# Kernel optimization log

Measured on AMD Instinct MI355X. Metric: run time of the kernel, lower is better.

Reference implementation:

```python
import jax, jax.numpy as jnp
import numpy as np

EPS = 1e-05


def project_to_poincare_ball(v, eps=EPS):
    # clip norm to < 1 - eps
    norm = jnp.linalg.norm(v, axis=-1, keepdims=True)
    scale = jnp.minimum((1.0 - eps) / (norm + 1e-10), 1.0)
    return v * scale


def setup_inputs() -> dict:
    key = jax.random.key(0)
    k1, k2 = jax.random.split(key)
    B, S, D, V = 2, 2048, 512, 32000
    # scale by 0.02 so typical norms (~0.45) lie inside the unit ball
    hidden_states = jax.random.normal(k1, (B, S, D), dtype=jnp.float32) * 0.02
    weight = jax.random.normal(k2, (V, D), dtype=jnp.float32) * 0.02
    return {"hidden_states": hidden_states, "weight": weight}


def reference(hidden_states, weight):
    eps = EPS
    B, S, D = hidden_states.shape
    x = hidden_states.reshape(-1, D)                 # (N, D)
    x = project_to_poincare_ball(x, eps)
    y = project_to_poincare_ball(weight, eps)        # (V, D)

    x_norm_sq = jnp.sum(x * x, axis=-1, keepdims=True)   # (N, 1)
    y_norm_sq = jnp.sum(y * y, axis=-1)                  # (V,)

    # torch.cdist(p=2, use_mm_for_euclid_dist): ||x-y|| via mm expansion,
    # clamped at 0 before sqrt. NOTE: original code names this diff_norm_sq
    # but it is the (unsquared) distance -- reproduced faithfully.
    sq = x_norm_sq + y_norm_sq[None, :] - 2.0 * (x @ y.T)   # (N, V)
    dist = jnp.sqrt(jnp.maximum(sq, 0.0))

    denom = (1.0 - x_norm_sq) * (1.0 - y_norm_sq)[None, :]  # (N, V)
    argument = 1.0 + 2.0 * dist / (denom + eps)
    argument = jnp.maximum(argument, 1.0 + eps)
    distances = jnp.arccosh(argument)                       # (N, V)

    logits = -distances
    return logits.reshape(B, S, -1)
```

## Files before the change

### kernel.cpp

```cpp
#include <hip/hip_runtime.h>
#include <hip/hip_bf16.h>

#define D_DIM 512
#define EPS 1e-5f
#define BM 256
#define BN 256
#define BK 32
#define KT 16

typedef __attribute__((ext_vector_type(8))) short bf16x8;
typedef __attribute__((ext_vector_type(4))) float f32x4;

__device__ __forceinline__ unsigned short f2bf(float f) {
  unsigned int u = __float_as_uint(f);
  u += 0x7FFFu + ((u >> 16) & 1u);
  return (unsigned short)(u >> 16);
}

__global__ __launch_bounds__(256) void prep_rows2(
    const float* __restrict__ x, const float* __restrict__ w,
    unsigned short* __restrict__ Xbf, unsigned short* __restrict__ Ybf,
    float* __restrict__ xnsq, float* __restrict__ ynsq, int N, int total)
{
  int row  = blockIdx.x * 4 + (threadIdx.x >> 6);
  int lane = threadIdx.x & 63;
  if (row >= total) return;

  const float* src; unsigned short* dst; float* nsq; int r;
  if (row < N) { src = x; dst = Xbf; nsq = xnsq; r = row; }
  else         { src = w; dst = Ybf; nsq = ynsq; r = row - N; }

  const float4* s = (const float4*)(src + (size_t)r * D_DIM);
  float4 v0 = s[lane];
  float4 v1 = s[lane + 64];
  float ss = v0.x*v0.x + v0.y*v0.y + v0.z*v0.z + v0.w*v0.w
           + v1.x*v1.x + v1.y*v1.y + v1.z*v1.z + v1.w*v1.w;
  #pragma unroll
  for (int off = 32; off; off >>= 1) ss += __shfl_xor(ss, off);

  float norm  = sqrtf(ss);
  float scale = fminf((1.0f - EPS) / (norm + 1e-10f), 1.0f);
  if (lane == 0) nsq[r] = ss * scale * scale;

  ushort4 o0, o1;
  o0.x = f2bf(v0.x * scale); o0.y = f2bf(v0.y * scale);
  o0.z = f2bf(v0.z * scale); o0.w = f2bf(v0.w * scale);
  o1.x = f2bf(v1.x * scale); o1.y = f2bf(v1.y * scale);
  o1.z = f2bf(v1.z * scale); o1.w = f2bf(v1.w * scale);

  ushort4* dp = (ushort4*)(dst + (size_t)r * D_DIM);
  dp[lane]      = o0;
  dp[lane + 64] = o1;
}

__global__ __launch_bounds__(512, 2) void hyp_gemm(
    const unsigned short* __restrict__ Xbf, const unsigned short* __restrict__ Ybf,
    const float* __restrict__ xnsq, const float* __restrict__ ynsq,
    float* __restrict__ out, int N, int V)
{
  __shared__ __attribute__((aligned(16))) unsigned short regions[2][2 * BM * BK];

  int bid = blockIdx.x;
  int local = bid >> 3;
  int bn = local >> 1;
  int bm = (bid & 7) * 2 + (local & 1);

  int tid  = threadIdx.x;
  int wid  = tid >> 6;
  int lane = tid & 63;
  int wm = wid >> 2, wn = wid & 3;

  size_t a_row0 = (size_t)bm * BM;
  size_t b_row0 = (size_t)bn * BN;

  int rA = tid >> 2;
  int sw = (tid & 3) ^ ((tid >> 2) & 3);
  auto STAGE = [&](int reg, int kt) {
    int k0 = kt * BK;
    char* base = (char*)&regions[reg][0];
    #pragma unroll
    for (int j = 0; j < 2; ++j) {
      const unsigned short* g = Xbf + (a_row0 + j * 128 + rA) * D_DIM + k0 + sw * 8;
      char* l = base + j * 8192 + wid * 1024;
      __builtin_amdgcn_global_load_lds(
          (const __attribute__((address_space(1))) void*)g,
          (__attribute__((address_space(3))) void*)l, 16, 0, 0);
    }
    #pragma unroll
    for (int j = 0; j < 2; ++j) {
      const unsigned short* g = Ybf + (b_row0 + j * 128 + rA) * D_DIM + k0 + sw * 8;
      char* l = base + 16384 + j * 8192 + wid * 1024;
      __builtin_amdgcn_global_load_lds(
          (const __attribute__((address_space(1))) void*)g,
          (__attribute__((address_space(3))) void*)l, 16, 0, 0);
    }
  };

  f32x4 acc[8][4] = {};
  int r = lane & 15;
  int h = lane >> 4;
  int slotoff = ((h ^ (r & 3)) * 8);

  STAGE(0, 0);

  #pragma unroll
  for (int t = 0; t < KT; ++t) {
    const unsigned short* sA = &regions[t & 1][0];
    const unsigned short* sB = sA + BM * BK;

    asm volatile("s_waitcnt vmcnt(0)" ::: "memory");
    __builtin_amdgcn_sched_barrier(0);
    __builtin_amdgcn_s_barrier();
    __builtin_amdgcn_sched_barrier(0);

    bf16x8 a[8], b0, b1;
    #pragma unroll
    for (int m = 0; m < 8; ++m)
      a[m] = *(const bf16x8*)&sA[(wm * 128 + m * 16 + r) * BK + slotoff];
    b0 = *(const bf16x8*)&sB[(wn * 64 + 0 * 16 + r) * BK + slotoff];
    b1 = *(const bf16x8*)&sB[(wn * 64 + 1 * 16 + r) * BK + slotoff];

    if (t + 1 < KT) STAGE((t + 1) & 1, t + 1);

    __builtin_amdgcn_sched_barrier(0);
    __builtin_amdgcn_s_barrier();
    __builtin_amdgcn_sched_barrier(0);
    __builtin_amdgcn_s_setprio(1);
    #pragma unroll
    for (int m = 0; m < 8; ++m) {
      acc[m][0] = __builtin_amdgcn_mfma_f32_16x16x32_bf16(b0, a[m], acc[m][0], 0, 0, 0);
      acc[m][1] = __builtin_amdgcn_mfma_f32_16x16x32_bf16(b1, a[m], acc[m][1], 0, 0, 0);
    }
    __builtin_amdgcn_s_setprio(0);

    __builtin_amdgcn_sched_barrier(0);
    __builtin_amdgcn_s_barrier();
    __builtin_amdgcn_sched_barrier(0);
    bf16x8 b2 = *(const bf16x8*)&sB[(wn * 64 + 2 * 16 + r) * BK + slotoff];
    bf16x8 b3 = *(const bf16x8*)&sB[(wn * 64 + 3 * 16 + r) * BK + slotoff];

    __builtin_amdgcn_sched_barrier(0);
    __builtin_amdgcn_s_barrier();
    __builtin_amdgcn_sched_barrier(0);
    __builtin_amdgcn_s_setprio(1);
    #pragma unroll
    for (int m = 0; m < 8; ++m) {
      acc[m][2] = __builtin_amdgcn_mfma_f32_16x16x32_bf16(b2, a[m], acc[m][2], 0, 0, 0);
      acc[m][3] = __builtin_amdgcn_mfma_f32_16x16x32_bf16(b3, a[m], acc[m][3], 0, 0, 0);
    }
    __builtin_amdgcn_s_setprio(0);
  }

  __syncthreads();
  float* epi = (float*)&regions[0][0] + wid * (16 * 68);

  int jr = r;
  float xnv[8], cmv[8];
  #pragma unroll
  for (int m = 0; m < 8; ++m) {
    float xn = xnsq[bm * BM + wm * 128 + m * 16 + jr];
    xnv[m] = xn;
    cmv[m] = 2.0f * __builtin_amdgcn_rcpf(1.0f - xn);
  }
  f32x4 ynv[4], rdy[4];
  #pragma unroll
  for (int n = 0; n < 4; ++n) {
    f32x4 y4 = *(const f32x4*)&ynsq[bn * BN + wn * 64 + n * 16 + h * 4];
    ynv[n] = y4;
    #pragma unroll
    for (int q = 0; q < 4; ++q) rdy[n][q] = __builtin_amdgcn_rcpf(1.0f - y4[q]);
  }

  size_t out_row0 = (size_t)bm * BM + wm * 128;
  int    out_col0 = bn * BN + wn * 64;

  #pragma unroll
  for (int m = 0; m < 8; ++m) {
    float xn = xnv[m], cm = cmv[m];
    #pragma unroll
    for (int n = 0; n < 4; ++n) {
      f32x4 f;
      #pragma unroll
      for (int q = 0; q < 4; ++q) {
        float dot  = acc[m][n][q];
        float sq   = fmaxf(xn + ynv[n][q] - 2.0f * dot, 0.0f);
        float dist = __builtin_amdgcn_sqrtf(sq);
        float arg  = fmaf(dist * cm, rdy[n][q], 1.0f);
        arg = fmaxf(arg, 1.0f + EPS);
        float t2 = __builtin_amdgcn_sqrtf(fmaf(arg, arg, -1.0f));
        f[q] = -__logf(arg + t2);
      }
      *(f32x4*)&epi[jr * 68 + n * 16 + h * 4] = f;
    }
    #pragma unroll
    for (int k = 0; k < 4; ++k) {
      int xl = k * 4 + h;
      f32x4 f = *(const f32x4*)&epi[xl * 68 + jr * 4];
      size_t rg = out_row0 + m * 16 + xl;
      int    cg = out_col0 + jr * 4;
      __builtin_nontemporal_store(f, (f32x4*)(out + rg * (size_t)V + cg));
    }
  }
}

extern "C" void kernel_launch(void* const* d_in, const int* in_sizes, int n_in,
                              void* d_out, int out_size, void* d_ws, size_t ws_size,
                              hipStream_t stream) {
  const float* x = (const float*)d_in[0];
  const float* w = (const float*)d_in[1];
  float* out = (float*)d_out;

  int N = in_sizes[0] / D_DIM;
  int V = in_sizes[1] / D_DIM;

  char* ws = (char*)d_ws;
  unsigned short* Xbf = (unsigned short*)ws;
  size_t xbf_bytes = (size_t)N * D_DIM * 2;
  unsigned short* Ybf = (unsigned short*)(ws + xbf_bytes);
  size_t ybf_bytes = (size_t)V * D_DIM * 2;
  float* xnsq = (float*)(ws + xbf_bytes + ybf_bytes);
  float* ynsq = xnsq + N;

  int total = N + V;
  prep_rows2<<<dim3((total + 3) / 4), dim3(256), 0, stream>>>(
      x, w, Xbf, Ybf, xnsq, ynsq, N, total);

  int nwg = (N / BM) * (V / BN);
  hyp_gemm<<<dim3(nwg), dim3(512), 0, stream>>>(Xbf, Ybf, xnsq, ynsq, out, N, V);
}
```

Measured before the change: 241.6 us.

## Triple-buffer LDS tiles with two-stage prefetch and split A/B staging

Moves the GEMM main loop from double to triple LDS buffering, prefetching the tile two steps ahead. Waits use a partial vmcnt so the tile in flight is not drained each iteration. The A and B staging loads are now issued at two separate points in the loop to spread memory traffic across the MFMA phases. Per-block LDS grows from 64 KB to 96 KB, so two 512-thread blocks may no longer fit on one CU, which can halve occupancy.

```diff
diff --git a/kernel.cpp b/kernel.cpp
--- a/kernel.cpp
+++ b/kernel.cpp
@@ -58,7 +58,7 @@
     const float* __restrict__ xnsq, const float* __restrict__ ynsq,
     float* __restrict__ out, int N, int V)
 {
-  __shared__ __attribute__((aligned(16))) unsigned short regions[2][2 * BM * BK];
+  __shared__ __attribute__((aligned(16))) unsigned short regions[3][2 * BM * BK];
 
   int bid = blockIdx.x;
   int local = bid >> 3;
@@ -73,23 +73,31 @@
   size_t a_row0 = (size_t)bm * BM;
   size_t b_row0 = (size_t)bn * BN;
 
-  int rA = tid >> 2;
-  int sw = (tid & 3) ^ ((tid >> 2) & 3);
-  auto STAGE = [&](int reg, int kt) {
+  auto STAGE_A = [&](int reg, int kt) {
     int k0 = kt * BK;
     char* base = (char*)&regions[reg][0];
     #pragma unroll
-    for (int j = 0; j < 2; ++j) {
-      const unsigned short* g = Xbf + (a_row0 + j * 128 + rA) * D_DIM + k0 + sw * 8;
-      char* l = base + j * 8192 + wid * 1024;
+    for (int i = 0; i < 2; ++i) {
+      int c = i * 512 + tid;
+      int row = c >> 2;
+      int sw = (c & 3) ^ (row & 3);
+      const unsigned short* g = Xbf + (a_row0 + row) * D_DIM + k0 + sw * 8;
+      char* l = base + (size_t)(i * 512 + wid * 64) * 16;
       __builtin_amdgcn_global_load_lds(
           (const __attribute__((address_space(1))) void*)g,
           (__attribute__((address_space(3))) void*)l, 16, 0, 0);
     }
-    #pragma unroll
-    for (int j = 0; j < 2; ++j) {
-      const unsigned short* g = Ybf + (b_row0 + j * 128 + rA) * D_DIM + k0 + sw * 8;
-      char* l = base + 16384 + j * 8192 + wid * 1024;
+  };
+  auto STAGE_B = [&](int reg, int kt) {
+    int k0 = kt * BK;
+    char* base = (char*)&regions[reg][0] + 2 * BM * BK;
+    #pragma unroll
+    for (int i = 0; i < 2; ++i) {
+      int c = i * 512 + tid;
+      int row = c >> 2;
+      int sw = (c & 3) ^ (row & 3);
+      const unsigned short* g = Ybf + (b_row0 + row) * D_DIM + k0 + sw * 8;
+      char* l = base + (size_t)(i * 512 + wid * 64) * 16;
       __builtin_amdgcn_global_load_lds(
           (const __attribute__((address_space(1))) void*)g,
           (__attribute__((address_space(3))) void*)l, 16, 0, 0);
@@ -99,16 +107,21 @@
   f32x4 acc[8][4] = {};
   int r = lane & 15;
   int h = lane >> 4;
-  int slotoff = ((h ^ (r & 3)) * 8);
-
-  STAGE(0, 0);
+  int slotoff = (h ^ (r & 3)) * 8;
+
+  STAGE_A(0, 0); STAGE_B(0, 0);
+  STAGE_A(1, 1); STAGE_B(1, 1);
 
   #pragma unroll
   for (int t = 0; t < KT; ++t) {
-    const unsigned short* sA = &regions[t & 1][0];
+    const unsigned short* sA = &regions[t % 3][0];
     const unsigned short* sB = sA + BM * BK;
 
-    asm volatile("s_waitcnt vmcnt(0)" ::: "memory");
+    if (t >= KT - 2) {
+      asm volatile("s_waitcnt vmcnt(0)" ::: "memory");
+    } else {
+      asm volatile("s_waitcnt vmcnt(4)" ::: "memory");
+    }
     __builtin_amdgcn_sched_barrier(0);
     __builtin_amdgcn_s_barrier();
     __builtin_amdgcn_sched_barrier(0);
@@ -119,8 +132,7 @@
       a[m] = *(const bf16x8*)&sA[(wm * 128 + m * 16 + r) * BK + slotoff];
     b0 = *(const bf16x8*)&sB[(wn * 64 + 0 * 16 + r) * BK + slotoff];
     b1 = *(const bf16x8*)&sB[(wn * 64 + 1 * 16 + r) * BK + slotoff];
-
-    if (t + 1 < KT) STAGE((t + 1) & 1, t + 1);
+    if (t + 2 < KT) STAGE_A((t + 2) % 3, t + 2);
 
     __builtin_amdgcn_sched_barrier(0);
     __builtin_amdgcn_s_barrier();
@@ -138,6 +150,7 @@
     __builtin_amdgcn_sched_barrier(0);
     bf16x8 b2 = *(const bf16x8*)&sB[(wn * 64 + 2 * 16 + r) * BK + slotoff];
     bf16x8 b3 = *(const bf16x8*)&sB[(wn * 64 + 3 * 16 + r) * BK + slotoff];
+    if (t + 2 < KT) STAGE_B((t + 2) % 3, t + 2);
 
     __builtin_amdgcn_sched_barrier(0);
     __builtin_amdgcn_s_barrier();
```

Result: no change. 239.1 us (-1.0%).
